# Kernel optimization log

Hardware: AMD Instinct MI355X
Metric: run time of the kernel (lower is better)

The kernel has to match this reference:

```python
import jax, jax.numpy as jnp
import numpy as np

NUM_CHR = 24
N_EMB = 512
DIM = 512
BATCH = 1024


def setup_inputs() -> dict:
    key = jax.random.key(0)
    k1, k2, k3 = jax.random.split(key, 3)
    chromosome = jax.random.randint(k1, (BATCH,), 0, NUM_CHR, dtype=jnp.int32)
    position = jax.random.uniform(k2, (BATCH, 1), dtype=jnp.float32)
    # Stacked per-chromosome parameters (ParameterDict -> stacked arrays)
    embeddings = jax.random.normal(k3, (NUM_CHR, N_EMB, DIM), dtype=jnp.float32)
    centers = jnp.broadcast_to(jnp.linspace(0.0, 1.0, N_EMB, dtype=jnp.float32), (NUM_CHR, N_EMB))
    log_variances = jnp.full((NUM_CHR, N_EMB), -2.0, dtype=jnp.float32)
    return {
        "chromosome": chromosome,
        "position": position,
        "embeddings": embeddings,
        "centers": centers,
        "log_variances": log_variances,
    }


def reference(chromosome, position, embeddings, centers, log_variances):
    # Gather per-sample chromosome parameter sets
    c = centers[chromosome]                     # [B, N]
    v = jnp.exp(log_variances[chromosome])      # [B, N]
    e = embeddings[chromosome]                  # [B, N, D]
    # Gaussian RBF weights over the chromosome's centers, normalized
    w = jnp.exp(-((position - c) ** 2) / (2.0 * v))  # [B, N] (position [B,1] broadcasts)
    w = w / jnp.sum(w, axis=1, keepdims=True)
    # Weighted sum of embeddings -> [B, D]
    return jnp.einsum("bn,bnd->bd", w, e)
```

## Files before the change

kernel.cpp:

```cpp
#include <hip/hip_runtime.h>

#define NUM_CHR 24
#define N_EMB   512
#define DIM     512
#define BATCH   1024

#define T_SAMP     16
#define GROUPS_CAP 6
#define NSPLIT_N   8
#define NCHUNK     (N_EMB / NSPLIT_N)
#define DSPLIT     2
#define DSLICE     (DIM / DSPLIT)

#define OFF_COUNTS 0u
#define OFF_LISTS  1024u
#define OFF_W      99328u
#define OFF_P      2196480u
#define P_BYTES    ((size_t)BATCH * DIM * sizeof(float))

__global__ __launch_bounds__(256) void atac_weights_kernel(
    const int* __restrict__ chrom, const float* __restrict__ pos,
    const float* __restrict__ centers, const float* __restrict__ logvar,
    float* __restrict__ W, int* __restrict__ counts, int* __restrict__ lists) {
  const int b = blockIdx.x;
  const int tid = threadIdx.x;
  const int c = chrom[b];
  const float p = pos[b];
  const int n0 = tid;
  const int n1 = tid + 256;
  const float* cc = centers + (size_t)c * N_EMB;
  const float* lv = logvar + (size_t)c * N_EMB;

  const float d0 = p - cc[n0];
  const float d1 = p - cc[n1];
  const float w0 = expf(-(d0 * d0) / (2.0f * expf(lv[n0])));
  const float w1 = expf(-(d1 * d1) / (2.0f * expf(lv[n1])));

  float s = w0 + w1;
#pragma unroll
  for (int off = 32; off > 0; off >>= 1) s += __shfl_down(s, off);
  __shared__ float part[4];
  __shared__ float invtot;
  if ((tid & 63) == 0) part[tid >> 6] = s;
  __syncthreads();
  if (tid == 0) invtot = 1.0f / (part[0] + part[1] + part[2] + part[3]);
  __syncthreads();

  float* Wb = W + (size_t)b * N_EMB;
  const float it = invtot;
  Wb[n0] = w0 * it;
  Wb[n1] = w1 * it;

  if (tid == 0) {
    const int slot = atomicAdd(&counts[c], 1);
    lists[c * BATCH + slot] = b;
  }
}

__global__ __launch_bounds__(256) void atac_reduce_kernel(
    const float* __restrict__ E, const float* __restrict__ W,
    const int* __restrict__ counts, const int* __restrict__ lists,
    float* __restrict__ P) {
  const int c = blockIdx.x;
  const int grp = blockIdx.y;
  const int zn = blockIdx.z & (NSPLIT_N - 1);
  const int zd = blockIdx.z >> 3;
  const int cnt = counts[c];
  const int base = grp * T_SAMP;
  if (base >= cnt) return;
  const int m = min(T_SAMP, cnt - base);
  const int tid = threadIdx.x;
  const int lane = tid & 63;
  const int sg = tid >> 6;
  const int sg4 = sg * 4;

  __shared__ int sidx[T_SAMP];
  __shared__ float wlT[NCHUNK][20];

  if (tid < T_SAMP) sidx[tid] = (tid < m) ? lists[c * BATCH + base + tid] : -1;
  __syncthreads();

  const int nbase = zn * NCHUNK;
  const int dbase = zd * DSLICE;

#pragma unroll
  for (int k = 0; k < 4; ++k) {
    const int idx = tid + k * 256;
    const int t = idx >> 6;
    const int j = idx & 63;
    const int s = sidx[t];
    wlT[j][t] = (s >= 0) ? W[(size_t)s * N_EMB + nbase + j] : 0.0f;
  }
  __syncthreads();

  float4 acc0 = make_float4(0.f, 0.f, 0.f, 0.f);
  float4 acc1 = acc0, acc2 = acc0, acc3 = acc0;

  const float* Eb = E + (size_t)c * (N_EMB * DIM) + (size_t)nbase * DIM + dbase + lane * 4;

  float4 e0 = *(const float4*)(Eb + 0 * DIM);
  float4 e1 = *(const float4*)(Eb + 1 * DIM);
  float4 e2 = *(const float4*)(Eb + 2 * DIM);
  float4 e3 = *(const float4*)(Eb + 3 * DIM);

#define FMA16(EV, WV)                         \
  acc0.x = fmaf(WV.x, EV.x, acc0.x);          \
  acc0.y = fmaf(WV.x, EV.y, acc0.y);          \
  acc0.z = fmaf(WV.x, EV.z, acc0.z);          \
  acc0.w = fmaf(WV.x, EV.w, acc0.w);          \
  acc1.x = fmaf(WV.y, EV.x, acc1.x);          \
  acc1.y = fmaf(WV.y, EV.y, acc1.y);          \
  acc1.z = fmaf(WV.y, EV.z, acc1.z);          \
  acc1.w = fmaf(WV.y, EV.w, acc1.w);          \
  acc2.x = fmaf(WV.z, EV.x, acc2.x);          \
  acc2.y = fmaf(WV.z, EV.y, acc2.y);          \
  acc2.z = fmaf(WV.z, EV.z, acc2.z);          \
  acc2.w = fmaf(WV.z, EV.w, acc2.w);          \
  acc3.x = fmaf(WV.w, EV.x, acc3.x);          \
  acc3.y = fmaf(WV.w, EV.y, acc3.y);          \
  acc3.z = fmaf(WV.w, EV.z, acc3.z);          \
  acc3.w = fmaf(WV.w, EV.w, acc3.w);

#pragma unroll 1
  for (int j = 0; j < NCHUNK; j += 4) {
    const bool more = (j + 4 < NCHUNK);
    const float* En = Eb + (size_t)(j + 4) * DIM;
    {
      const float4 wv = *(const float4*)&wlT[j + 0][sg4];
      FMA16(e0, wv)
      if (more) e0 = *(const float4*)(En + 0 * DIM);
    }
    {
      const float4 wv = *(const float4*)&wlT[j + 1][sg4];
      FMA16(e1, wv)
      if (more) e1 = *(const float4*)(En + 1 * DIM);
    }
    {
      const float4 wv = *(const float4*)&wlT[j + 2][sg4];
      FMA16(e2, wv)
      if (more) e2 = *(const float4*)(En + 2 * DIM);
    }
    {
      const float4 wv = *(const float4*)&wlT[j + 3][sg4];
      FMA16(e3, wv)
      if (more) e3 = *(const float4*)(En + 3 * DIM);
    }
  }
#undef FMA16

  float* Pz = P + (size_t)zn * (BATCH * DIM) + dbase + lane * 4;
  if (sg4 + 0 < m) *(float4*)(Pz + (size_t)sidx[sg4 + 0] * DIM) = acc0;
  if (sg4 + 1 < m) *(float4*)(Pz + (size_t)sidx[sg4 + 1] * DIM) = acc1;
  if (sg4 + 2 < m) *(float4*)(Pz + (size_t)sidx[sg4 + 2] * DIM) = acc2;
  if (sg4 + 3 < m) *(float4*)(Pz + (size_t)sidx[sg4 + 3] * DIM) = acc3;
}

__global__ __launch_bounds__(256) void atac_final_reduce(
    const float* __restrict__ P, float* __restrict__ out) {
  const int i = blockIdx.x * 256 + threadIdx.x;
  const float4* p = (const float4*)P;
  float4 s = p[i];
#pragma unroll
  for (int zz = 1; zz < NSPLIT_N; ++zz) {
    const float4 v = p[(size_t)zz * (BATCH * DIM / 4) + i];
    s.x += v.x; s.y += v.y; s.z += v.z; s.w += v.w;
  }
  ((float4*)out)[i] = s;
}

__global__ __launch_bounds__(512) void atac_fused_naive(
    const int* __restrict__ chrom, const float* __restrict__ pos,
    const float* __restrict__ E, const float* __restrict__ centers,
    const float* __restrict__ logvar, float* __restrict__ out) {
  const int b = blockIdx.x;
  const int tid = threadIdx.x;
  const int c = chrom[b];
  const float p = pos[b];
  __shared__ float w[N_EMB];
  __shared__ float red[8];

  const float d = p - centers[(size_t)c * N_EMB + tid];
  const float wv = expf(-(d * d) / (2.0f * expf(logvar[(size_t)c * N_EMB + tid])));
  float s = wv;
#pragma unroll
  for (int off = 32; off > 0; off >>= 1) s += __shfl_down(s, off);
  if ((tid & 63) == 0) red[tid >> 6] = s;
  __syncthreads();
  if (tid == 0) {
    float tot = 0.f;
#pragma unroll
    for (int i = 0; i < 8; ++i) tot += red[i];
    red[0] = 1.0f / tot;
  }
  __syncthreads();
  w[tid] = wv * red[0];
  __syncthreads();

  float acc = 0.f;
  const float* Ec = E + (size_t)c * (N_EMB * DIM) + tid;
  for (int n = 0; n < N_EMB; ++n) acc = fmaf(w[n], Ec[(size_t)n * DIM], acc);
  out[(size_t)b * DIM + tid] = acc;
}

extern "C" void kernel_launch(void* const* d_in, const int* in_sizes, int n_in,
                              void* d_out, int out_size, void* d_ws, size_t ws_size,
                              hipStream_t stream) {
  const int* chrom = (const int*)d_in[0];
  const float* pos = (const float*)d_in[1];
  const float* E = (const float*)d_in[2];
  const float* centers = (const float*)d_in[3];
  const float* logvar = (const float*)d_in[4];
  float* out = (float*)d_out;
  char* ws = (char*)d_ws;

  if (ws_size < OFF_P + (size_t)NSPLIT_N * P_BYTES) {
    atac_fused_naive<<<BATCH, 512, 0, stream>>>(chrom, pos, E, centers, logvar, out);
    return;
  }

  int* counts = (int*)(ws + OFF_COUNTS);
  int* lists = (int*)(ws + OFF_LISTS);
  float* W = (float*)(ws + OFF_W);
  float* P = (float*)(ws + OFF_P);

  hipMemsetAsync(counts, 0, NUM_CHR * sizeof(int), stream);
  atac_weights_kernel<<<BATCH, 256, 0, stream>>>(chrom, pos, centers, logvar, W,
                                                 counts, lists);
  atac_reduce_kernel<<<dim3(NUM_CHR, GROUPS_CAP, NSPLIT_N * DSPLIT), 256, 0, stream>>>(
      E, W, counts, lists, P);
  atac_final_reduce<<<(BATCH * DIM / 4) / 256, 256, 0, stream>>>(P, out);
}
```

Measured before the change: 107.7 us.

## Stage embedding rows into LDS with double-buffered direct global-to-LDS loads

The reduce kernel no longer has each wave load the same embedding rows into registers itself. Instead the block loads 8-row chunks once into a double-buffered shared-memory tile through global_load_lds, and every wave then reads the shared tile. This removes the four-fold duplicated global loads across the four waves and overlaps prefetch of the next chunk with compute. In exchange it adds a barrier per chunk and more LDS traffic, and correctness depends on the global_load_lds layout matching the 16-byte-per-lane addressing.

```diff
diff --git a/kernel.cpp b/kernel.cpp
--- a/kernel.cpp
+++ b/kernel.cpp
@@ -11,6 +11,8 @@
 #define NCHUNK     (N_EMB / NSPLIT_N)
 #define DSPLIT     2
 #define DSLICE     (DIM / DSPLIT)
+#define RCHUNK     8
+#define NCHUNKS    (NCHUNK / RCHUNK)
 
 #define OFF_COUNTS 0u
 #define OFF_LISTS  1024u
@@ -76,6 +78,7 @@
 
   __shared__ int sidx[T_SAMP];
   __shared__ float wlT[NCHUNK][20];
+  __shared__ float ebuf[2][RCHUNK][DSLICE];
 
   if (tid < T_SAMP) sidx[tid] = (tid < m) ? lists[c * BATCH + base + tid] : -1;
   __syncthreads();
@@ -87,21 +90,29 @@
   for (int k = 0; k < 4; ++k) {
     const int idx = tid + k * 256;
     const int t = idx >> 6;
-    const int j = idx & 63;
+    const int j = idx & (NCHUNK - 1);
     const int s = sidx[t];
     wlT[j][t] = (s >= 0) ? W[(size_t)s * N_EMB + nbase + j] : 0.0f;
   }
-  __syncthreads();
+
+  const float* Eb = E + (size_t)c * (N_EMB * DIM) + (size_t)nbase * DIM + dbase;
+
+#define STAGE(NB, CK)                                                          \
+  {                                                                            \
+    const float* g0 = Eb + (size_t)((CK) * RCHUNK + sg * 2) * DIM + lane * 4;  \
+    __builtin_amdgcn_global_load_lds(                                          \
+        (const __attribute__((address_space(1))) unsigned int*)g0,             \
+        (__attribute__((address_space(3))) unsigned int*)&ebuf[NB][sg * 2][0], \
+        16, 0, 0);                                                             \
+    const float* g1 = g0 + DIM;                                                \
+    __builtin_amdgcn_global_load_lds(                                          \
+        (const __attribute__((address_space(1))) unsigned int*)g1,             \
+        (__attribute__((address_space(3))) unsigned int*)&ebuf[NB][sg * 2 + 1][0], \
+        16, 0, 0);                                                             \
+  }
 
   float4 acc0 = make_float4(0.f, 0.f, 0.f, 0.f);
   float4 acc1 = acc0, acc2 = acc0, acc3 = acc0;
-
-  const float* Eb = E + (size_t)c * (N_EMB * DIM) + (size_t)nbase * DIM + dbase + lane * 4;
-
-  float4 e0 = *(const float4*)(Eb + 0 * DIM);
-  float4 e1 = *(const float4*)(Eb + 1 * DIM);
-  float4 e2 = *(const float4*)(Eb + 2 * DIM);
-  float4 e3 = *(const float4*)(Eb + 3 * DIM);
 
 #define FMA16(EV, WV)                         \
   acc0.x = fmaf(WV.x, EV.x, acc0.x);          \
@@ -121,32 +132,24 @@
   acc3.z = fmaf(WV.w, EV.z, acc3.z);          \
   acc3.w = fmaf(WV.w, EV.w, acc3.w);
 
+  STAGE(0, 0);
+  __syncthreads();
+
+  int cur = 0;
 #pragma unroll 1
-  for (int j = 0; j < NCHUNK; j += 4) {
-    const bool more = (j + 4 < NCHUNK);
-    const float* En = Eb + (size_t)(j + 4) * DIM;
-    {
-      const float4 wv = *(const float4*)&wlT[j + 0][sg4];
-      FMA16(e0, wv)
-      if (more) e0 = *(const float4*)(En + 0 * DIM);
+  for (int ck = 0; ck < NCHUNKS; ++ck) {
+    if (ck + 1 < NCHUNKS) STAGE(cur ^ 1, ck + 1);
+#pragma unroll
+    for (int r = 0; r < RCHUNK; ++r) {
+      const float4 e = *(const float4*)&ebuf[cur][r][lane * 4];
+      const float4 wv = *(const float4*)&wlT[ck * RCHUNK + r][sg4];
+      FMA16(e, wv)
     }
-    {
-      const float4 wv = *(const float4*)&wlT[j + 1][sg4];
-      FMA16(e1, wv)
-      if (more) e1 = *(const float4*)(En + 1 * DIM);
-    }
-    {
-      const float4 wv = *(const float4*)&wlT[j + 2][sg4];
-      FMA16(e2, wv)
-      if (more) e2 = *(const float4*)(En + 2 * DIM);
-    }
-    {
-      const float4 wv = *(const float4*)&wlT[j + 3][sg4];
-      FMA16(e3, wv)
-      if (more) e3 = *(const float4*)(En + 3 * DIM);
-    }
+    __syncthreads();
+    cur ^= 1;
   }
 #undef FMA16
+#undef STAGE
 
   float* Pz = P + (size_t)zn * (BATCH * DIM) + dbase + lane * 4;
   if (sg4 + 0 < m) *(float4*)(Pz + (size_t)sidx[sg4 + 0] * DIM) = acc0;
```

New measurement: 104.2 us. -3.2%, faster.
